# Performance work log

Measured on AMD Instinct MI355X. Metric: run time of the kernel, lower is better.

The kernel has to match this reference:

```python
import jax, jax.numpy as jnp
import numpy as np

DEPTH = 100
HIDDEN = 1024
SHIFT = 25  # number of zeros prepended by the Shift module
LINEARITY = 0.97


def setup_inputs() -> dict:
    key = jax.random.key(0)
    ks = jax.random.split(key, 9)
    IN, OUT, B = 512, 512, 4096
    x = jax.random.normal(ks[0], (B, IN), dtype=jnp.float32)
    # torch Linear weight shape: [out, in]; xavier/kaiming init approximated by scaled normals
    fc1_w = jax.random.normal(ks[1], (HIDDEN, IN), dtype=jnp.float32) * (1.0 / np.sqrt(IN))
    fc1_b = jnp.zeros((HIDDEN,), dtype=jnp.float32)
    W1 = jax.random.normal(ks[2], (DEPTH, HIDDEN, HIDDEN), dtype=jnp.float32) * (1.0 / np.sqrt(HIDDEN))
    b1 = jnp.zeros((DEPTH, HIDDEN), dtype=jnp.float32)
    W2 = jax.random.normal(ks[3], (DEPTH, HIDDEN, HIDDEN), dtype=jnp.float32) * (np.sqrt(2.0) / np.sqrt(HIDDEN))
    b2 = jnp.zeros((DEPTH, HIDDEN), dtype=jnp.float32)
    fc2_w = jax.random.normal(ks[4], (OUT, HIDDEN), dtype=jnp.float32) * (1.0 / np.sqrt(HIDDEN))
    fc2_b = jnp.zeros((OUT,), dtype=jnp.float32)
    return {"x": x, "fc1_w": fc1_w, "fc1_b": fc1_b, "W1": W1, "b1": b1,
            "W2": W2, "b2": b2, "fc2_w": fc2_w, "fc2_b": fc2_b}


def _shift(x):
    # Shift: cat 25 zeros in front along last dim, then slice back to original width
    z = jnp.zeros_like(x[..., :SHIFT])
    return jnp.concatenate([z, x[..., :-SHIFT]], axis=-1)


def reference(x, fc1_w, fc1_b, W1, b1, W2, b2, fc2_w, fc2_b):
    x = x @ fc1_w.T + fc1_b  # [B, HIDDEN]

    def block(h, params):
        w1, bb1, w2, bb2 = params
        r = _shift(h)                       # shifted input is the residual
        a = jnp.maximum(r @ w1.T + bb1, 0)  # fc1 + clamp(min=0)
        y = a @ w2.T + bb2                  # fc2
        out = LINEARITY * r + (1.0 - LINEARITY) * y
        return out, None

    x, _ = jax.lax.scan(block, x, (W1, b1, W2, b2))
    return x @ fc2_w.T + fc2_b
```

## Files before the change

### kernel.cpp

```cpp
#include <hip/hip_runtime.h>
#include <cstdint>
#include <cstddef>

#define DEPTH 100
#define HID 1024
#define MROWS 4096
#define NSTEPS 202

typedef _Float16 half8 __attribute__((ext_vector_type(8)));
typedef float floatx4 __attribute__((ext_vector_type(4)));

__device__ __forceinline__ void gload_lds16_a(const void* g, void* l) {
    __builtin_amdgcn_global_load_lds((const __attribute__((address_space(1))) void*)g,
                                     (__attribute__((address_space(3))) void*)l, 16, 0, 1);
}
__device__ __forceinline__ void gload_lds16_w(const void* g, void* l) {
    __builtin_amdgcn_global_load_lds((const __attribute__((address_space(1))) void*)g,
                                     (__attribute__((address_space(3))) void*)l, 16, 0, 2);
}
__device__ __forceinline__ float ld_sc0_f32(const float* p) {
    return __hip_atomic_load(p, __ATOMIC_RELAXED, __HIP_MEMORY_SCOPE_AGENT);
}

__global__ __launch_bounds__(512, 1)
void resnet_persist(const _Float16* __restrict__ xh, const _Float16* __restrict__ fc1h,
                    const float* __restrict__ fc1_b,
                    const _Float16* __restrict__ W1h, const float* __restrict__ b1,
                    const _Float16* __restrict__ W2h, const float* __restrict__ b2,
                    const _Float16* __restrict__ fc2h, const float* __restrict__ fc2_b,
                    float* __restrict__ Sst, _Float16* __restrict__ rb,
                    _Float16* __restrict__ ab, float* __restrict__ outp,
                    unsigned* __restrict__ ctr)
{
    __shared__ _Float16 As[3][128 * 64];
    __shared__ _Float16 Bs[3][128 * 64];
    __shared__ float    Ht[128 * 128];

    const int tid = threadIdx.x;
    const int l   = tid & 63;
    const int w   = tid >> 6;
    const int wm  = w >> 2;
    const int wn  = w & 3;

    const int lr = l >> 3;
    const int lj = l & 7;
    const int sw = (l & 7) << 4;

    unsigned xcd_s;
    asm volatile("s_getreg_b32 %0, hwreg(HW_REG_XCC_ID)" : "=s"(xcd_s));
    unsigned* shm = (unsigned*)Ht;
    if (tid == 0) {
        const unsigned x = xcd_s & 7u;
        const unsigned r = __hip_atomic_fetch_add(&ctr[x * 32], 1u, __ATOMIC_RELAXED, __HIP_MEMORY_SCOPE_AGENT);
        __hip_atomic_fetch_add(&ctr[8 * 32], 1u, __ATOMIC_RELEASE, __HIP_MEMORY_SCOPE_AGENT);
        while (__hip_atomic_load(&ctr[8 * 32], __ATOMIC_RELAXED, __HIP_MEMORY_SCOPE_AGENT) < 256u)
            __builtin_amdgcn_s_sleep(2);
        __builtin_amdgcn_fence(__ATOMIC_ACQUIRE, "agent");
        unsigned ok = 1u;
        for (int i2 = 0; i2 < 8; ++i2)
            ok &= (__hip_atomic_load(&ctr[i2 * 32], __ATOMIC_RELAXED, __HIP_MEMORY_SCOPE_AGENT) == 32u) ? 1u : 0u;
        shm[0] = r; shm[1] = ok; shm[2] = x;
    }
    __syncthreads();
    const unsigned rank  = shm[0];
    const unsigned okf   = shm[1];
    const unsigned myxcd = shm[2];
    __syncthreads();

    const float C1 = 0.97f;
    const float C2 = (float)(1.0 - 0.97);
    const size_t SBUF = (size_t)32 * 9 * 128 * 25;

    for (int s = 0; s < NSTEPS; ++s) {
        if (s > 0) {
            asm volatile("s_waitcnt vmcnt(0) lgkmcnt(0)" ::: "memory");
            __syncthreads();
            if (okf) {
                if (tid == 0) {
                    unsigned* slot = &ctr[(1024 + ((s - 1) * 8 + (int)myxcd)) * 32];
                    __hip_atomic_fetch_add(slot, 1u, __ATOMIC_RELAXED, __HIP_MEMORY_SCOPE_AGENT);
                    while (__hip_atomic_load(slot, __ATOMIC_RELAXED, __HIP_MEMORY_SCOPE_AGENT) < 32u)
                        __builtin_amdgcn_s_sleep(2);
                }
                __syncthreads();
                __builtin_amdgcn_sched_barrier(0);
            } else {
                if (tid == 0) {
                    unsigned* slot = &ctr[(1024 + 2048 + (s - 1)) * 32];
                    __hip_atomic_fetch_add(slot, 1u, __ATOMIC_RELEASE, __HIP_MEMORY_SCOPE_AGENT);
                    while (__hip_atomic_load(slot, __ATOMIC_RELAXED, __HIP_MEMORY_SCOPE_AGENT) < 256u)
                        __builtin_amdgcn_s_sleep(4);
                }
                __syncthreads();
                __builtin_amdgcn_fence(__ATOMIC_ACQUIRE, "agent");
            }
        }

        const _Float16* A; const _Float16* B; const float* bias;
        int K, mode, rshift = 0, rbuf = 0, wbuf = 0;
        if (s == 0) {
            A = xh; B = fc1h; bias = fc1_b; K = 512; mode = 0;
            rshift = 25; wbuf = 0;
        } else if (s == NSTEPS - 1) {
            A = rb; B = fc2h; bias = fc2_b; K = HID; mode = 3;
        } else {
            const int d = (s - 1) >> 1;
            if (s & 1) {
                A = rb; B = W1h + (size_t)d * HID * HID; bias = b1 + d * HID;
                K = HID; mode = 1;
            } else {
                A = ab; B = W2h + (size_t)d * HID * HID; bias = b2 + d * HID;
                K = HID; mode = 2;
                rbuf = d & 1; wbuf = 1 - rbuf;
                rshift = (d == DEPTH - 1) ? 0 : 25;
            }
        }

        int bm, bn; bool active = true;
        if (okf) {
            if (mode == 3) {
                if (rank < 16u) { bm = (int)myxcd * 4 + (int)(rank >> 2); bn = (int)(rank & 3u); }
                else { active = false; bm = 0; bn = 0; }
            } else {
                bm = (int)myxcd * 4 + (int)(rank >> 3); bn = (int)(rank & 7u);
            }
        } else {
            const int b0  = blockIdx.x;
            const int bid = (b0 & 7) * 32 + (b0 >> 3);
            if (mode == 3) {
                if (bid < 128) { bm = bid >> 2; bn = bid & 3; }
                else { active = false; bm = 0; bn = 0; }
            } else {
                bm = bid >> 3; bn = bid & 7;
            }
        }
        if (!active) continue;

        floatx4 acc[4][2];
        const floatx4 zero = {0.f, 0.f, 0.f, 0.f};
        #pragma unroll
        for (int i = 0; i < 4; ++i)
            #pragma unroll
            for (int j = 0; j < 2; ++j) acc[i][j] = zero;

        auto stage = [&](int buf, int kt) {
            #pragma unroll
            for (int q = 0; q < 2; ++q) {
                const int c   = w * 2 + q;
                const int row = c * 8 + lr;
                const int jch = lj ^ (row & 7);
                gload_lds16_w((const void*)(B + (size_t)(bn * 128 + row) * K + kt * 64 + jch * 8),
                              (void*)((char*)Bs[buf] + c * 1024));
            }
            #pragma unroll
            for (int q = 0; q < 2; ++q) {
                const int c   = w * 2 + q;
                const int row = c * 8 + lr;
                const int jch = lj ^ (row & 7);
                gload_lds16_a((const void*)(A + (size_t)(bm * 128 + row) * K + kt * 64 + jch * 8),
                              (void*)((char*)As[buf] + c * 1024));
            }
        };

        auto compute = [&](int buf) {
            #pragma unroll
            for (int kk = 0; kk < 2; ++kk) {
                half8 af[4], bf[2];
                #pragma unroll
                for (int fi = 0; fi < 4; ++fi) {
                    const int off = ((wm * 64 + fi * 16 + (l & 15)) * 128 + kk * 64 + ((l >> 4) << 4)) ^ sw;
                    af[fi] = *(const half8*)((const char*)As[buf] + off);
                }
                #pragma unroll
                for (int fj = 0; fj < 2; ++fj) {
                    const int off = ((wn * 32 + fj * 16 + (l & 15)) * 128 + kk * 64 + ((l >> 4) << 4)) ^ sw;
                    bf[fj] = *(const half8*)((const char*)Bs[buf] + off);
                }
                __builtin_amdgcn_s_setprio(1);
                #pragma unroll
                for (int fi = 0; fi < 4; ++fi)
                    #pragma unroll
                    for (int fj = 0; fj < 2; ++fj)
                        acc[fi][fj] = __builtin_amdgcn_mfma_f32_16x16x32_f16(af[fi], bf[fj], acc[fi][fj], 0, 0, 0);
                __builtin_amdgcn_s_setprio(0);
            }
        };

        const int nkt = K >> 6;
        stage(0, 0);
        stage(1, 1);
        int cur = 0;
        for (int kt = 0; kt < nkt; ++kt) {
            if (kt + 2 < nkt) {
                int n2 = cur + 2; if (n2 >= 3) n2 -= 3;
                stage(n2, kt + 2);
            }
            const int rem   = nkt - 1 - kt;
            const int ahead = rem < 2 ? rem : 2;
            if (ahead == 2)      asm volatile("s_waitcnt vmcnt(8)" ::: "memory");
            else if (ahead == 1) asm volatile("s_waitcnt vmcnt(4)" ::: "memory");
            else                 asm volatile("s_waitcnt vmcnt(0)" ::: "memory");
            __builtin_amdgcn_s_barrier();
            __builtin_amdgcn_sched_barrier(0);
            compute(cur);
            __builtin_amdgcn_s_barrier();
            cur = (cur + 1 == 3) ? 0 : cur + 1;
        }

        const int colb = bn * 128 + wn * 32 + (l & 15);
        const int rowb = bm * 128 + wm * 64 + ((l >> 4) << 2);
        const int jl0  = wn * 32 + (l & 15);
        const int il0  = wm * 64 + ((l >> 4) << 2);

        if (mode == 1) {
            #pragma unroll
            for (int fi = 0; fi < 4; ++fi)
                #pragma unroll
                for (int fj = 0; fj < 2; ++fj) {
                    const int j = colb + fj * 16;
                    const float bj = bias[j];
                    #pragma unroll
                    for (int v = 0; v < 4; ++v)
                        ab[(size_t)(rowb + fi * 16 + v) * HID + j] = (_Float16)fmaxf(acc[fi][fj][v] + bj, 0.f);
                }
        } else if (mode == 3) {
            #pragma unroll
            for (int fi = 0; fi < 4; ++fi)
                #pragma unroll
                for (int fj = 0; fj < 2; ++fj) {
                    const int j = colb + fj * 16;
                    const float bj = bias[j];
                    #pragma unroll
                    for (int v = 0; v < 4; ++v)
                        outp[(size_t)(rowb + fi * 16 + v) * 512 + j] = acc[fi][fj][v] + bj;
                }
        } else {
            float rv[4][2][4];
            if (mode == 2) {
                const float* Srd = Sst + (size_t)rbuf * SBUF + ((size_t)(bm * 9 + bn) * 128) * 25;
                #pragma unroll
                for (int fi = 0; fi < 4; ++fi)
                    #pragma unroll
                    for (int fj = 0; fj < 2; ++fj) {
                        const int jl = jl0 + fj * 16;
                        #pragma unroll
                        for (int v = 0; v < 4; ++v) {
                            const int il = il0 + fi * 16 + v;
                            if (jl >= 25)      rv[fi][fj][v] = Ht[il * 128 + (jl - 25)];
                            else if (bn > 0)   rv[fi][fj][v] = ld_sc0_f32(Srd + il * 25 + jl);
                            else               rv[fi][fj][v] = 0.f;
                        }
                    }
                __syncthreads();
            }
            float* Swr = Sst + (size_t)wbuf * SBUF + ((size_t)(bm * 9 + bn + 1) * 128) * 25;
            #pragma unroll
            for (int fi = 0; fi < 4; ++fi)
                #pragma unroll
                for (int fj = 0; fj < 2; ++fj) {
                    const int j  = colb + fj * 16;
                    const int jl = jl0 + fj * 16;
                    const float bj = bias[j];
                    #pragma unroll
                    for (int v = 0; v < 4; ++v) {
                        const int i  = rowb + fi * 16 + v;
                        const int il = il0 + fi * 16 + v;
                        const float val = acc[fi][fj][v] + bj;
                        const float hv = (mode == 2) ? (C1 * rv[fi][fj][v] + C2 * val) : val;
                        Ht[il * 128 + jl] = hv;
                        if (rshift == 0) {
                            rb[(size_t)i * HID + j] = (_Float16)hv;
                        } else {
                            const int jd = j + 25;
                            if (jd < HID) rb[(size_t)i * HID + jd] = (_Float16)hv;
                            if (j < 25)   rb[(size_t)i * HID + j]  = (_Float16)0.f;
                            if (jl >= 103) Swr[il * 25 + (jl - 103)] = hv;
                        }
                    }
                }
        }
    }
}

__global__ void cvt_kernel(const float* __restrict__ in, _Float16* __restrict__ out, long n8)
{
    const long stride = (long)gridDim.x * 256;
    for (long idx = (long)blockIdx.x * 256 + threadIdx.x; idx < n8; idx += stride) {
        const floatx4 f0 = ((const floatx4*)in)[idx * 2];
        const floatx4 f1 = ((const floatx4*)in)[idx * 2 + 1];
        half8 h;
        #pragma unroll
        for (int i = 0; i < 4; ++i) {
            h[i]     = (_Float16)f0[i];
            h[4 + i] = (_Float16)f1[i];
        }
        ((half8*)out)[idx] = h;
    }
}

__global__ void zero_ctr(unsigned* __restrict__ ctr, int n)
{
    const int i = blockIdx.x * 256 + threadIdx.x;
    if (i < n) ctr[i] = 0u;
}

static inline void launch_cvt(const float* in, _Float16* out, long n, hipStream_t s)
{
    const long n8 = n / 8;
    int blocks = (int)((n8 + 255) / 256);
    if (blocks > 2048) blocks = 2048;
    cvt_kernel<<<dim3(blocks), dim3(256), 0, s>>>(in, out, n8);
}

extern "C" void kernel_launch(void* const* d_in, const int* in_sizes, int n_in,
                              void* d_out, int out_size, void* d_ws, size_t ws_size,
                              hipStream_t stream)
{
    (void)in_sizes; (void)n_in; (void)out_size; (void)ws_size;
    const float* x     = (const float*)d_in[0];
    const float* fc1_w = (const float*)d_in[1];
    const float* fc1_b = (const float*)d_in[2];
    const float* W1    = (const float*)d_in[3];
    const float* b1    = (const float*)d_in[4];
    const float* W2    = (const float*)d_in[5];
    const float* b2    = (const float*)d_in[6];
    const float* fc2_w = (const float*)d_in[7];
    const float* fc2_b = (const float*)d_in[8];
    float* out = (float*)d_out;

    char* ws = (char*)d_ws;
    _Float16* xh   = (_Float16*)(ws);
    _Float16* rb   = (_Float16*)(ws + (4ull   << 20));
    _Float16* ab   = (_Float16*)(ws + (12ull  << 20));
    _Float16* fc1h = (_Float16*)(ws + (52ull  << 20));
    _Float16* fc2h = (_Float16*)(ws + (53ull  << 20));
    _Float16* W1h  = (_Float16*)(ws + (54ull  << 20));
    _Float16* W2h  = (_Float16*)(ws + (254ull << 20));
    unsigned* ctr  = (unsigned*)(ws + (460ull << 20));
    float*    Sst  = (float*)   (ws + (468ull << 20));

    launch_cvt(x, xh, (long)MROWS * 512, stream);
    launch_cvt(fc1_w, fc1h, (long)HID * 512, stream);
    launch_cvt(W1,    W1h,  (long)DEPTH * HID * HID, stream);
    launch_cvt(W2,    W2h,  (long)DEPTH * HID * HID, stream);
    launch_cvt(fc2_w, fc2h, (long)512 * HID, stream);
    zero_ctr<<<dim3(512), dim3(256), 0, stream>>>(ctr, 131072);

    resnet_persist<<<dim3(256), dim3(512), 0, stream>>>(
        xh, fc1h, fc1_b, W1h, b1, W2h, b2, fc2h, fc2_b,
        Sst, rb, ab, out, ctr);
}
```

Measured before the change: 5.037 ms.

## Stage activation tiles through registers with double-buffered LDS instead of direct global-to-LDS loads

The A-operand (activation) tiles are now loaded into registers with sc0 global loads and written to a two-slot LDS buffer one step ahead. Weights keep the triple-buffered direct global-to-LDS path. This likely targets the cache coherence behaviour of the activation loads, which are produced by other blocks, and saves one LDS A buffer. In exchange it adds register pressure, extra LDS write instructions and more waitcnt ordering in the main loop. The Sst workspace offset also moves.

```diff
diff --git a/kernel.cpp b/kernel.cpp
--- a/kernel.cpp
+++ b/kernel.cpp
@@ -9,14 +9,16 @@
 
 typedef _Float16 half8 __attribute__((ext_vector_type(8)));
 typedef float floatx4 __attribute__((ext_vector_type(4)));
-
-__device__ __forceinline__ void gload_lds16_a(const void* g, void* l) {
-    __builtin_amdgcn_global_load_lds((const __attribute__((address_space(1))) void*)g,
-                                     (__attribute__((address_space(3))) void*)l, 16, 0, 1);
-}
+typedef unsigned uintx4 __attribute__((ext_vector_type(4)));
+
 __device__ __forceinline__ void gload_lds16_w(const void* g, void* l) {
     __builtin_amdgcn_global_load_lds((const __attribute__((address_space(1))) void*)g,
                                      (__attribute__((address_space(3))) void*)l, 16, 0, 2);
+}
+__device__ __forceinline__ uintx4 gload16_sc0(const void* p) {
+    uintx4 r;
+    asm volatile("global_load_dwordx4 %0, %1, off sc0" : "=v"(r) : "v"(p) : "memory");
+    return r;
 }
 __device__ __forceinline__ float ld_sc0_f32(const float* p) {
     return __hip_atomic_load(p, __ATOMIC_RELAXED, __HIP_MEMORY_SCOPE_AGENT);
@@ -32,7 +34,7 @@
                     _Float16* __restrict__ ab, float* __restrict__ outp,
                     unsigned* __restrict__ ctr)
 {
-    __shared__ _Float16 As[3][128 * 64];
+    __shared__ _Float16 Adb[2][128 * 64];
     __shared__ _Float16 Bs[3][128 * 64];
     __shared__ float    Ht[128 * 128];
 
@@ -71,6 +73,9 @@
     const float C2 = (float)(1.0 - 0.97);
     const size_t SBUF = (size_t)32 * 9 * 128 * 25;
 
+    const int dd0 = (w * 2 + 0) * 1024 + lr * 128 + ((lj ^ lr) << 4);
+    const int dd1 = (w * 2 + 1) * 1024 + lr * 128 + ((lj ^ lr) << 4);
+
     for (int s = 0; s < NSTEPS; ++s) {
         if (s > 0) {
             asm volatile("s_waitcnt vmcnt(0) lgkmcnt(0)" ::: "memory");
@@ -83,7 +88,6 @@
                         __builtin_amdgcn_s_sleep(2);
                 }
                 __syncthreads();
-                __builtin_amdgcn_sched_barrier(0);
             } else {
                 if (tid == 0) {
                     unsigned* slot = &ctr[(1024 + 2048 + (s - 1)) * 32];
@@ -94,6 +98,7 @@
                 __syncthreads();
                 __builtin_amdgcn_fence(__ATOMIC_ACQUIRE, "agent");
             }
+            __builtin_amdgcn_sched_barrier(0);
         }
 
         const _Float16* A; const _Float16* B; const float* bias;
@@ -143,7 +148,12 @@
             #pragma unroll
             for (int j = 0; j < 2; ++j) acc[i][j] = zero;
 
-        auto stage = [&](int buf, int kt) {
+        const char* a0p = (const char*)A +
+            2 * ((size_t)(bm * 128 + (w * 2 + 0) * 8 + lr) * K + lj * 8);
+        const char* a1p = (const char*)A +
+            2 * ((size_t)(bm * 128 + (w * 2 + 1) * 8 + lr) * K + lj * 8);
+
+        auto stageB = [&](int buf, int kt) {
             #pragma unroll
             for (int q = 0; q < 2; ++q) {
                 const int c   = w * 2 + q;
@@ -152,24 +162,16 @@
                 gload_lds16_w((const void*)(B + (size_t)(bn * 128 + row) * K + kt * 64 + jch * 8),
                               (void*)((char*)Bs[buf] + c * 1024));
             }
-            #pragma unroll
-            for (int q = 0; q < 2; ++q) {
-                const int c   = w * 2 + q;
-                const int row = c * 8 + lr;
-                const int jch = lj ^ (row & 7);
-                gload_lds16_a((const void*)(A + (size_t)(bm * 128 + row) * K + kt * 64 + jch * 8),
-                              (void*)((char*)As[buf] + c * 1024));
-            }
         };
 
-        auto compute = [&](int buf) {
+        auto compute = [&](int abuf, int buf) {
             #pragma unroll
             for (int kk = 0; kk < 2; ++kk) {
                 half8 af[4], bf[2];
                 #pragma unroll
                 for (int fi = 0; fi < 4; ++fi) {
                     const int off = ((wm * 64 + fi * 16 + (l & 15)) * 128 + kk * 64 + ((l >> 4) << 4)) ^ sw;
-                    af[fi] = *(const half8*)((const char*)As[buf] + off);
+                    af[fi] = *(const half8*)((const char*)Adb[abuf] + off);
                 }
                 #pragma unroll
                 for (int fj = 0; fj < 2; ++fj) {
@@ -187,22 +189,39 @@
         };
 
         const int nkt = K >> 6;
-        stage(0, 0);
-        stage(1, 1);
+        uintx4 aR0, aR1;
+
+        aR0 = gload16_sc0((const void*)a0p);
+        aR1 = gload16_sc0((const void*)a1p);
+        asm volatile("s_waitcnt vmcnt(0)" ::: "memory");
+        *(uintx4*)((char*)Adb[0] + dd0) = aR0;
+        *(uintx4*)((char*)Adb[0] + dd1) = aR1;
+        stageB(0, 0);
+        aR0 = gload16_sc0((const void*)(a0p + 128));
+        aR1 = gload16_sc0((const void*)(a1p + 128));
+        stageB(1, 1);
+        asm volatile("s_waitcnt lgkmcnt(0)" ::: "memory");
+
         int cur = 0;
         for (int kt = 0; kt < nkt; ++kt) {
-            if (kt + 2 < nkt) {
-                int n2 = cur + 2; if (n2 >= 3) n2 -= 3;
-                stage(n2, kt + 2);
-            }
-            const int rem   = nkt - 1 - kt;
-            const int ahead = rem < 2 ? rem : 2;
-            if (ahead == 2)      asm volatile("s_waitcnt vmcnt(8)" ::: "memory");
-            else if (ahead == 1) asm volatile("s_waitcnt vmcnt(4)" ::: "memory");
-            else                 asm volatile("s_waitcnt vmcnt(0)" ::: "memory");
+            if (kt + 1 < nkt) asm volatile("s_waitcnt vmcnt(4)" ::: "memory");
+            else              asm volatile("s_waitcnt vmcnt(0)" ::: "memory");
             __builtin_amdgcn_s_barrier();
             __builtin_amdgcn_sched_barrier(0);
-            compute(cur);
+            if (kt + 1 < nkt) {
+                asm volatile("s_waitcnt vmcnt(2)" ::: "memory");
+                const int ab2 = (kt + 1) & 1;
+                *(uintx4*)((char*)Adb[ab2] + dd0) = aR0;
+                *(uintx4*)((char*)Adb[ab2] + dd1) = aR1;
+            }
+            if (kt + 2 < nkt) {
+                aR0 = gload16_sc0((const void*)(a0p + (size_t)(kt + 2) * 128));
+                aR1 = gload16_sc0((const void*)(a1p + (size_t)(kt + 2) * 128));
+                int n2 = cur + 2; if (n2 >= 3) n2 -= 3;
+                stageB(n2, kt + 2);
+            }
+            compute(kt & 1, cur);
+            asm volatile("s_waitcnt lgkmcnt(0)" ::: "memory");
             __builtin_amdgcn_s_barrier();
             cur = (cur + 1 == 3) ? 0 : cur + 1;
         }
@@ -337,7 +356,7 @@
     _Float16* W1h  = (_Float16*)(ws + (54ull  << 20));
     _Float16* W2h  = (_Float16*)(ws + (254ull << 20));
     unsigned* ctr  = (unsigned*)(ws + (460ull << 20));
-    float*    Sst  = (float*)   (ws + (468ull << 20));
+    float*    Sst  = (float*)   (ws + (462ull << 20));
 
     launch_cvt(x, xh, (long)MROWS * 512, stream);
     launch_cvt(fc1_w, fc1h, (long)HID * 512, stream);
```

Result: no change. 4.956 ms (-1.6%).
